# Performance work log

Hardware: AMD Instinct MI355X
Metric: run time of the kernel (lower is better)

Reference implementation:

```python
import jax, jax.numpy as jnp
import numpy as np

TOP_K = 2


def setup_inputs() -> dict:
    key = jax.random.key(0)
    ks = jax.random.split(key, 8)
    B, S, H, I, E = 1, 1024, 2048, 1408, 8
    s = 0.02  # init scale for weights
    return {
        "hidden_states": jax.random.normal(ks[0], (B, S, H), jnp.float32),
        "gate_weight": jax.random.normal(ks[1], (E, H), jnp.float32) * s,
        "expert_gate_w": jax.random.normal(ks[2], (E, I, H), jnp.float32) * s,
        "expert_up_w": jax.random.normal(ks[3], (E, I, H), jnp.float32) * s,
        "expert_down_w": jax.random.normal(ks[4], (E, H, I), jnp.float32) * s,
        "shared_gate_w": jax.random.normal(ks[5], (I, H), jnp.float32) * s,
        "shared_up_w": jax.random.normal(ks[6], (I, H), jnp.float32) * s,
        "shared_down_w": jax.random.normal(ks[7], (H, I), jnp.float32) * s,
    }


def reference(hidden_states, gate_weight, expert_gate_w, expert_up_w, expert_down_w,
              shared_gate_w, shared_up_w, shared_down_w):
    B, S, H = hidden_states.shape
    E = gate_weight.shape[0]
    x = hidden_states.reshape(-1, H)          # [T, H]
    T = x.shape[0]

    # --- gate: top-k routing (e_score_correction_bias buffer is zeros -> no-op) ---
    logits = x @ gate_weight.T                # [T, E]
    topk_logits, topk_idx = jax.lax.top_k(logits, TOP_K)
    topk_w = jax.nn.softmax(topk_logits, axis=-1)  # [T, K]

    # per-token per-expert combine weight (0 for non-selected experts) [T, E]
    comb = jnp.zeros((T, E), x.dtype).at[jnp.arange(T)[:, None], topk_idx].add(topk_w)

    # --- routed experts: dense over E, weighted combine (mathematically identical
    # to the per-token loop since comb==0 for unselected experts) ---
    g = jnp.einsum('th,eih->tei', x, expert_gate_w)   # [T, E, I]
    u = jnp.einsum('th,eih->tei', x, expert_up_w)     # [T, E, I]
    h = jax.nn.silu(g) * u                            # [T, E, I]
    y = jnp.einsum('tei,ehi->teh', h, expert_down_w)  # [T, E, H]
    out = jnp.einsum('teh,te->th', y, comb)           # [T, H]

    # --- shared expert ---
    sh = (jax.nn.silu(x @ shared_gate_w.T) * (x @ shared_up_w.T)) @ shared_down_w.T
    out = out + sh
    return out.reshape(B, S, H)
```

## Files before the change

kernel.cpp:

```cpp
#include <hip/hip_runtime.h>
#include <hip/hip_bf16.h>

typedef unsigned short u16;
typedef __bf16 bf16x8 __attribute__((ext_vector_type(8)));
typedef float f32x4 __attribute__((ext_vector_type(4)));

#define H_DIM 2048
#define I_DIM 1408
#define T_TOK 1024
#define NEXP 8
#define LS 40

__device__ __forceinline__ u16 f2bf(float f) {
    union { float f; unsigned u; } v; v.f = f;
    unsigned r = v.u + 0x7FFFu + ((v.u >> 16) & 1u);
    return (u16)(r >> 16);
}
__device__ __forceinline__ unsigned pack2(float a, float b) {
    float2 t; t.x = a; t.y = b;
    __hip_bfloat162 h = __float22bfloat162_rn(t);
    union { __hip_bfloat162 h; unsigned u; } v; v.h = h;
    return v.u;
}
__device__ __forceinline__ uint2 pack4(float4 f) {
    uint2 r; r.x = pack2(f.x, f.y); r.y = pack2(f.z, f.w); return r;
}

__global__ __launch_bounds__(256)
void router_kernel(const float* __restrict__ x, const float* __restrict__ gw,
                   int* __restrict__ counts, int* __restrict__ tok, float* __restrict__ tw) {
    int wave = threadIdx.x >> 6;
    int lane = threadIdx.x & 63;
    int t = blockIdx.x * 4 + wave;
    const float* xr = x + (size_t)t * H_DIM;
    float acc[NEXP];
#pragma unroll
    for (int e = 0; e < NEXP; e++) acc[e] = 0.f;
    for (int h = lane; h < H_DIM; h += 64) {
        float xv = xr[h];
#pragma unroll
        for (int e = 0; e < NEXP; e++) acc[e] += xv * gw[e * H_DIM + h];
    }
#pragma unroll
    for (int e = 0; e < NEXP; e++) {
#pragma unroll
        for (int off = 32; off > 0; off >>= 1) acc[e] += __shfl_xor(acc[e], off);
    }
    if (lane == 0) {
        int i0 = 0; float v0 = acc[0];
#pragma unroll
        for (int e = 1; e < NEXP; e++) if (acc[e] > v0) { v0 = acc[e]; i0 = e; }
        int i1 = -1; float v1 = -3.0e38f;
#pragma unroll
        for (int e = 0; e < NEXP; e++) if (e != i0 && acc[e] > v1) { v1 = acc[e]; i1 = e; }
        float ex = __expf(v1 - v0);
        float w0 = 1.f / (1.f + ex);
        float w1 = 1.f - w0;
        int s0 = atomicAdd(&counts[i0], 1);
        tok[i0 * T_TOK + s0] = t; tw[i0 * T_TOK + s0] = w0;
        int s1 = atomicAdd(&counts[i1], 1);
        tok[i1 * T_TOK + s1] = t; tw[i1 * T_TOK + s1] = w1;
    }
}

__global__ __launch_bounds__(256, 2)
void gate_up_kernel(const float* __restrict__ x,
                    const float* __restrict__ egw, const float* __restrict__ euw,
                    const float* __restrict__ sgw, const float* __restrict__ suw,
                    const int* __restrict__ counts, const int* __restrict__ tok,
                    const float* __restrict__ tw,
                    u16* __restrict__ h_r, u16* __restrict__ h_s) {
    __shared__ u16 lA[64 * LS];
    __shared__ u16 lG[128 * LS];
    __shared__ u16 lU[128 * LS];

    int e = blockIdx.z;
    bool routed = (e < NEXP);
    int cnt, hbase;
    const float *Wg, *Wu; u16* hout;
    if (routed) {
        cnt = counts[e];
        int p = 0;
#pragma unroll
        for (int i = 0; i < NEXP; i++) { int c = counts[i]; if (i < e) p += c; }
        hbase = p;
        Wg = egw + (size_t)e * I_DIM * H_DIM;
        Wu = euw + (size_t)e * I_DIM * H_DIM;
        hout = h_r;
    } else {
        cnt = T_TOK; hbase = 0; Wg = sgw; Wu = suw; hout = h_s;
    }
    int m0 = blockIdx.y * 64;
    if (m0 >= cnt) return;
    int n0 = blockIdx.x * 128;

    int tid = threadIdx.x;
    int lane = tid & 63;
    int w = tid >> 6;

    const float* ap[2]; int sa[2];
#pragma unroll
    for (int i = 0; i < 2; i++) {
        int slot = tid + i * 256;
        int row = slot >> 3, c4 = slot & 7;
        sa[i] = row * LS + c4 * 4;
        int trow = m0 + row; if (trow > cnt - 1) trow = cnt - 1;
        int tix = routed ? tok[e * T_TOK + trow] : trow;
        ap[i] = x + (size_t)tix * H_DIM + c4 * 4;
    }
    const float* gp[4]; const float* up[4]; int sg[4];
#pragma unroll
    for (int i = 0; i < 4; i++) {
        int slot = tid + i * 256;
        int row = slot >> 3, c4 = slot & 7;
        sg[i] = row * LS + c4 * 4;
        gp[i] = Wg + (size_t)(n0 + row) * H_DIM + c4 * 4;
        up[i] = Wu + (size_t)(n0 + row) * H_DIM + c4 * 4;
    }

    f32x4 zero = {0.f, 0.f, 0.f, 0.f};
    f32x4 accg[4][2], accu[4][2];
#pragma unroll
    for (int a = 0; a < 4; a++)
#pragma unroll
        for (int b = 0; b < 2; b++) { accg[a][b] = zero; accu[a][b] = zero; }

    int r16 = lane & 15, kq = lane >> 4;

    float4 ra[2], rg[4], ru[4];
#pragma unroll
    for (int i = 0; i < 2; i++) ra[i] = *(const float4*)(ap[i]);
#pragma unroll
    for (int i = 0; i < 4; i++) { rg[i] = *(const float4*)(gp[i]); ru[i] = *(const float4*)(up[i]); }

    for (int k0 = 0; k0 < H_DIM; k0 += 32) {
#pragma unroll
        for (int i = 0; i < 2; i++) *(uint2*)&lA[sa[i]] = pack4(ra[i]);
#pragma unroll
        for (int i = 0; i < 4; i++) {
            *(uint2*)&lG[sg[i]] = pack4(rg[i]);
            *(uint2*)&lU[sg[i]] = pack4(ru[i]);
        }
        __syncthreads();
        if (k0 + 32 < H_DIM) {
            int kn = k0 + 32;
#pragma unroll
            for (int i = 0; i < 2; i++) ra[i] = *(const float4*)(ap[i] + kn);
#pragma unroll
            for (int i = 0; i < 4; i++) { rg[i] = *(const float4*)(gp[i] + kn); ru[i] = *(const float4*)(up[i] + kn); }
        }
        bf16x8 af[4], gf[2], uf[2];
#pragma unroll
        for (int mi = 0; mi < 4; mi++)
            af[mi] = *(const bf16x8*)&lA[(mi * 16 + r16) * LS + kq * 8];
#pragma unroll
        for (int ni = 0; ni < 2; ni++) {
            gf[ni] = *(const bf16x8*)&lG[(w * 32 + ni * 16 + r16) * LS + kq * 8];
            uf[ni] = *(const bf16x8*)&lU[(w * 32 + ni * 16 + r16) * LS + kq * 8];
        }
#pragma unroll
        for (int mi = 0; mi < 4; mi++)
#pragma unroll
            for (int ni = 0; ni < 2; ni++) {
                accg[mi][ni] = __builtin_amdgcn_mfma_f32_16x16x32_bf16(af[mi], gf[ni], accg[mi][ni], 0, 0, 0);
                accu[mi][ni] = __builtin_amdgcn_mfma_f32_16x16x32_bf16(af[mi], uf[ni], accu[mi][ni], 0, 0, 0);
            }
        __syncthreads();
    }

#pragma unroll
    for (int mi = 0; mi < 4; mi++) {
#pragma unroll
        for (int r = 0; r < 4; r++) {
            int row = mi * 16 + kq * 4 + r;
            int gr = m0 + row;
            if (gr < cnt) {
                float wt = routed ? tw[e * T_TOK + gr] : 1.0f;
                u16* hrow = hout + (size_t)(hbase + gr) * I_DIM + n0 + w * 32;
#pragma unroll
                for (int ni = 0; ni < 2; ni++) {
                    float g = accg[mi][ni][r], u = accu[mi][ni][r];
                    float hv = (g / (1.f + __expf(-g))) * u * wt;
                    hrow[ni * 16 + r16] = f2bf(hv);
                }
            }
        }
    }
}

__global__ __launch_bounds__(256, 2)
void down_kernel(const u16* __restrict__ h_r, const u16* __restrict__ h_s,
                 const float* __restrict__ edw, const float* __restrict__ sdw,
                 const int* __restrict__ counts, const int* __restrict__ tok,
                 float* __restrict__ out) {
    __shared__ u16 lA[64 * LS];
    __shared__ u16 lB[128 * LS];

    int e = blockIdx.z;
    bool routed = (e < NEXP);
    int cnt, hbase;
    const float* Wd; const u16* hin;
    if (routed) {
        cnt = counts[e];
        int p = 0;
#pragma unroll
        for (int i = 0; i < NEXP; i++) { int c = counts[i]; if (i < e) p += c; }
        hbase = p;
        Wd = edw + (size_t)e * H_DIM * I_DIM;
        hin = h_r;
    } else {
        cnt = T_TOK; hbase = 0; Wd = sdw; hin = h_s;
    }
    int m0 = blockIdx.y * 64;
    if (m0 >= cnt) return;
    int n0 = blockIdx.x * 128;

    int tid = threadIdx.x;
    int lane = tid & 63;
    int w = tid >> 6;

    int arow = tid >> 2, ac8 = tid & 3;
    int hr = m0 + arow; if (hr > cnt - 1) hr = cnt - 1;
    const u16* ap = hin + (size_t)(hbase + hr) * I_DIM + ac8 * 8;
    int sa = arow * LS + ac8 * 8;
    const float* bp[4]; int sb[4];
#pragma unroll
    for (int i = 0; i < 4; i++) {
        int slot = tid + i * 256;
        int row = slot >> 3, c4 = slot & 7;
        bp[i] = Wd + (size_t)(n0 + row) * I_DIM + c4 * 4;
        sb[i] = row * LS + c4 * 4;
    }

    f32x4 zero = {0.f, 0.f, 0.f, 0.f};
    f32x4 acc[4][2];
#pragma unroll
    for (int a = 0; a < 4; a++)
#pragma unroll
        for (int b = 0; b < 2; b++) acc[a][b] = zero;

    int r16 = lane & 15, kq = lane >> 4;

    uint4 ra = *(const uint4*)(ap);
    float4 rb[4];
#pragma unroll
    for (int i = 0; i < 4; i++) rb[i] = *(const float4*)(bp[i]);

    for (int k0 = 0; k0 < I_DIM; k0 += 32) {
        *(uint4*)&lA[sa] = ra;
#pragma unroll
        for (int i = 0; i < 4; i++) *(uint2*)&lB[sb[i]] = pack4(rb[i]);
        __syncthreads();
        if (k0 + 32 < I_DIM) {
            int kn = k0 + 32;
            ra = *(const uint4*)(ap + kn);
#pragma unroll
            for (int i = 0; i < 4; i++) rb[i] = *(const float4*)(bp[i] + kn);
        }
        bf16x8 af[4], bfr[2];
#pragma unroll
        for (int mi = 0; mi < 4; mi++)
            af[mi] = *(const bf16x8*)&lA[(mi * 16 + r16) * LS + kq * 8];
#pragma unroll
        for (int ni = 0; ni < 2; ni++)
            bfr[ni] = *(const bf16x8*)&lB[(w * 32 + ni * 16 + r16) * LS + kq * 8];
#pragma unroll
        for (int mi = 0; mi < 4; mi++)
#pragma unroll
            for (int ni = 0; ni < 2; ni++)
                acc[mi][ni] = __builtin_amdgcn_mfma_f32_16x16x32_bf16(af[mi], bfr[ni], acc[mi][ni], 0, 0, 0);
        __syncthreads();
    }

#pragma unroll
    for (int mi = 0; mi < 4; mi++) {
#pragma unroll
        for (int r = 0; r < 4; r++) {
            int row = mi * 16 + kq * 4 + r;
            int gr = m0 + row;
            if (gr < cnt) {
                int t = routed ? tok[e * T_TOK + gr] : gr;
                float* orow = out + (size_t)t * H_DIM + n0 + w * 32;
#pragma unroll
                for (int ni = 0; ni < 2; ni++)
                    atomicAdd(&orow[ni * 16 + r16], acc[mi][ni][r]);
            }
        }
    }
}

extern "C" void kernel_launch(void* const* d_in, const int* in_sizes, int n_in,
                              void* d_out, int out_size, void* d_ws, size_t ws_size,
                              hipStream_t stream) {
    const float* x   = (const float*)d_in[0];
    const float* gw  = (const float*)d_in[1];
    const float* egw = (const float*)d_in[2];
    const float* euw = (const float*)d_in[3];
    const float* edw = (const float*)d_in[4];
    const float* sgw = (const float*)d_in[5];
    const float* suw = (const float*)d_in[6];
    const float* sdw = (const float*)d_in[7];
    float* out = (float*)d_out;

    char* ws = (char*)d_ws;
    int*   counts = (int*)ws;
    int*   tok    = (int*)(ws + 256);
    float* tw     = (float*)(ws + 256 + 32768);
    u16*   h_r    = (u16*)(ws + 65792);
    u16*   h_s    = h_r + (size_t)2048 * I_DIM;

    hipMemsetAsync(counts, 0, 32, stream);
    hipMemsetAsync(out, 0, (size_t)T_TOK * H_DIM * sizeof(float), stream);
    router_kernel<<<256, 256, 0, stream>>>(x, gw, counts, tok, tw);
    gate_up_kernel<<<dim3(11, 16, 9), 256, 0, stream>>>(x, egw, euw, sgw, suw, counts, tok, tw, h_r, h_s);
    down_kernel<<<dim3(16, 16, 9), 256, 0, stream>>>(h_r, h_s, edw, sdw, counts, tok, out);
}
```

Measured before the change: 543.2 us.

## Pre-convert weights to bf16 and stage GEMM tiles via direct global-to-LDS loads

Adds a conversion kernel that casts all expert and shared weights plus activations to bf16 in workspace every call. New gate/up and down kernels then load bf16 tiles straight into LDS with global_load_lds, using an XOR-swizzled layout and K=64 steps, and target 3 blocks per CU. The intent is to halve the bytes the GEMMs read and remove the per-tile register conversion. The cost is an extra full pass that reads the fp32 weights and writes bf16 copies, which may cancel the saving because the weights are only used once per call. The old fp32 path stays as a fallback when the workspace is too small.

New measurement: 523.7 us. 1.04x faster.

```diff
diff --git a/kernel.cpp b/kernel.cpp
--- a/kernel.cpp
+++ b/kernel.cpp
@@ -24,6 +24,10 @@
 }
 __device__ __forceinline__ uint2 pack4(float4 f) {
     uint2 r; r.x = pack2(f.x, f.y); r.y = pack2(f.z, f.w); return r;
+}
+__device__ __forceinline__ void g2l16(const void* g, void* l) {
+    __builtin_amdgcn_global_load_lds((const __attribute__((address_space(1))) void*)g,
+                                     (__attribute__((address_space(3))) void*)l, 16, 0, 0);
 }
 
 __global__ __launch_bounds__(256)
@@ -63,21 +67,35 @@
     }
 }
 
-__global__ __launch_bounds__(256, 2)
-void gate_up_kernel(const float* __restrict__ x,
-                    const float* __restrict__ egw, const float* __restrict__ euw,
-                    const float* __restrict__ sgw, const float* __restrict__ suw,
-                    const int* __restrict__ counts, const int* __restrict__ tok,
-                    const float* __restrict__ tw,
-                    u16* __restrict__ h_r, u16* __restrict__ h_s) {
-    __shared__ u16 lA[64 * LS];
-    __shared__ u16 lG[128 * LS];
-    __shared__ u16 lU[128 * LS];
+struct Cvt7 { const float* in[7]; u16* out[7]; int nchunk[7]; };
+__global__ __launch_bounds__(256)
+void convert_bf(Cvt7 a) {
+    int z = blockIdx.z;
+    int n = a.nchunk[z];
+    const float* in = a.in[z]; u16* out = a.out[z];
+    for (int i = blockIdx.x * 256 + threadIdx.x; i < n; i += gridDim.x * 256) {
+        const float4* p = (const float4*)(in + (size_t)i * 8);
+        float4 f0 = p[0], f1 = p[1];
+        uint4 o; o.x = pack2(f0.x, f0.y); o.y = pack2(f0.z, f0.w);
+        o.z = pack2(f1.x, f1.y); o.w = pack2(f1.z, f1.w);
+        *(uint4*)(out + (size_t)i * 8) = o;
+    }
+}
+
+__global__ __launch_bounds__(256, 3)
+void gate_up_bf(const u16* __restrict__ xb,
+                const u16* __restrict__ egw, const u16* __restrict__ euw,
+                const u16* __restrict__ sgw, const u16* __restrict__ suw,
+                const int* __restrict__ counts, const int* __restrict__ tok,
+                const float* __restrict__ tw,
+                u16* __restrict__ h_r, u16* __restrict__ h_s) {
+    __shared__ u16 lA[64 * 64];
+    __shared__ u16 lG[128 * 64];
+    __shared__ u16 lU[128 * 64];
 
     int e = blockIdx.z;
     bool routed = (e < NEXP);
-    int cnt, hbase;
-    const float *Wg, *Wu; u16* hout;
+    int cnt, hbase; const u16 *Wg, *Wu; u16* hout;
     if (routed) {
         cnt = counts[e];
         int p = 0;
@@ -87,17 +105,225 @@
         Wg = egw + (size_t)e * I_DIM * H_DIM;
         Wu = euw + (size_t)e * I_DIM * H_DIM;
         hout = h_r;
-    } else {
-        cnt = T_TOK; hbase = 0; Wg = sgw; Wu = suw; hout = h_s;
-    }
+    } else { cnt = T_TOK; hbase = 0; Wg = sgw; Wu = suw; hout = h_s; }
     int m0 = blockIdx.y * 64;
     if (m0 >= cnt) return;
     int n0 = blockIdx.x * 128;
 
-    int tid = threadIdx.x;
-    int lane = tid & 63;
-    int w = tid >> 6;
-
+    int tid = threadIdx.x, lane = tid & 63, w = tid >> 6;
+
+    const u16* aptr[2]; u16* alds[2];
+#pragma unroll
+    for (int j = 0; j < 2; j++) {
+        int chunk = w * 128 + j * 64 + lane;
+        int row = chunk >> 3, cl = chunk & 7;
+        int cg = cl ^ (row & 7);
+        int trow = m0 + row; if (trow > cnt - 1) trow = cnt - 1;
+        int tix = routed ? tok[e * T_TOK + trow] : trow;
+        aptr[j] = xb + (size_t)tix * H_DIM + cg * 8;
+        alds[j] = &lA[(w * 128 + j * 64) * 8];
+    }
+    const u16* gptr[4]; const u16* uptr[4]; u16* glds[4]; u16* ulds[4];
+#pragma unroll
+    for (int j = 0; j < 4; j++) {
+        int chunk = w * 256 + j * 64 + lane;
+        int row = chunk >> 3, cl = chunk & 7;
+        int cg = cl ^ (row & 7);
+        gptr[j] = Wg + (size_t)(n0 + row) * H_DIM + cg * 8;
+        uptr[j] = Wu + (size_t)(n0 + row) * H_DIM + cg * 8;
+        glds[j] = &lG[(w * 256 + j * 64) * 8];
+        ulds[j] = &lU[(w * 256 + j * 64) * 8];
+    }
+
+    f32x4 zero = {0.f, 0.f, 0.f, 0.f};
+    f32x4 accg[4][2], accu[4][2];
+#pragma unroll
+    for (int a = 0; a < 4; a++)
+#pragma unroll
+        for (int b = 0; b < 2; b++) { accg[a][b] = zero; accu[a][b] = zero; }
+
+    int r16 = lane & 15, q = lane >> 4;
+
+    for (int k0 = 0; k0 < H_DIM; k0 += 64) {
+#pragma unroll
+        for (int j = 0; j < 2; j++) g2l16(aptr[j] + k0, alds[j]);
+#pragma unroll
+        for (int j = 0; j < 4; j++) { g2l16(gptr[j] + k0, glds[j]); g2l16(uptr[j] + k0, ulds[j]); }
+        __syncthreads();
+#pragma unroll
+        for (int kh = 0; kh < 2; kh++) {
+            bf16x8 af[4], gf[2], uf[2];
+#pragma unroll
+            for (int mi = 0; mi < 4; mi++) {
+                int row = mi * 16 + r16;
+                int ch = (kh * 4 + q) ^ (row & 7);
+                af[mi] = *(const bf16x8*)&lA[row * 64 + ch * 8];
+            }
+#pragma unroll
+            for (int ni = 0; ni < 2; ni++) {
+                int row = w * 32 + ni * 16 + r16;
+                int ch = (kh * 4 + q) ^ (row & 7);
+                gf[ni] = *(const bf16x8*)&lG[row * 64 + ch * 8];
+                uf[ni] = *(const bf16x8*)&lU[row * 64 + ch * 8];
+            }
+#pragma unroll
+            for (int mi = 0; mi < 4; mi++)
+#pragma unroll
+                for (int ni = 0; ni < 2; ni++) {
+                    accg[mi][ni] = __builtin_amdgcn_mfma_f32_16x16x32_bf16(af[mi], gf[ni], accg[mi][ni], 0, 0, 0);
+                    accu[mi][ni] = __builtin_amdgcn_mfma_f32_16x16x32_bf16(af[mi], uf[ni], accu[mi][ni], 0, 0, 0);
+                }
+        }
+        __syncthreads();
+    }
+
+#pragma unroll
+    for (int mi = 0; mi < 4; mi++) {
+#pragma unroll
+        for (int r = 0; r < 4; r++) {
+            int row = mi * 16 + q * 4 + r;
+            int gr = m0 + row;
+            if (gr < cnt) {
+                float wt = routed ? tw[e * T_TOK + gr] : 1.0f;
+                u16* hrow = hout + (size_t)(hbase + gr) * I_DIM + n0 + w * 32;
+#pragma unroll
+                for (int ni = 0; ni < 2; ni++) {
+                    float g = accg[mi][ni][r], u = accu[mi][ni][r];
+                    float hv = (g / (1.f + __expf(-g))) * u * wt;
+                    hrow[ni * 16 + r16] = f2bf(hv);
+                }
+            }
+        }
+    }
+}
+
+__global__ __launch_bounds__(256, 3)
+void down_bf(const u16* __restrict__ h_r, const u16* __restrict__ h_s,
+             const u16* __restrict__ edw, const u16* __restrict__ sdw,
+             const int* __restrict__ counts, const int* __restrict__ tok,
+             float* __restrict__ out) {
+    __shared__ u16 lA[64 * 64];
+    __shared__ u16 lB[128 * 64];
+
+    int e = blockIdx.z;
+    bool routed = (e < NEXP);
+    int cnt, hbase; const u16* Wd; const u16* hin;
+    if (routed) {
+        cnt = counts[e];
+        int p = 0;
+#pragma unroll
+        for (int i = 0; i < NEXP; i++) { int c = counts[i]; if (i < e) p += c; }
+        hbase = p;
+        Wd = edw + (size_t)e * H_DIM * I_DIM;
+        hin = h_r;
+    } else { cnt = T_TOK; hbase = 0; Wd = sdw; hin = h_s; }
+    int m0 = blockIdx.y * 64;
+    if (m0 >= cnt) return;
+    int n0 = blockIdx.x * 128;
+
+    int tid = threadIdx.x, lane = tid & 63, w = tid >> 6;
+
+    const u16* aptr[2]; u16* alds[2];
+#pragma unroll
+    for (int j = 0; j < 2; j++) {
+        int chunk = w * 128 + j * 64 + lane;
+        int row = chunk >> 3, cl = chunk & 7;
+        int cg = cl ^ (row & 7);
+        int hr = m0 + row; if (hr > cnt - 1) hr = cnt - 1;
+        aptr[j] = hin + (size_t)(hbase + hr) * I_DIM + cg * 8;
+        alds[j] = &lA[(w * 128 + j * 64) * 8];
+    }
+    const u16* bptr[4]; u16* blds[4];
+#pragma unroll
+    for (int j = 0; j < 4; j++) {
+        int chunk = w * 256 + j * 64 + lane;
+        int row = chunk >> 3, cl = chunk & 7;
+        int cg = cl ^ (row & 7);
+        bptr[j] = Wd + (size_t)(n0 + row) * I_DIM + cg * 8;
+        blds[j] = &lB[(w * 256 + j * 64) * 8];
+    }
+
+    f32x4 zero = {0.f, 0.f, 0.f, 0.f};
+    f32x4 acc[4][2];
+#pragma unroll
+    for (int a = 0; a < 4; a++)
+#pragma unroll
+        for (int b = 0; b < 2; b++) acc[a][b] = zero;
+
+    int r16 = lane & 15, q = lane >> 4;
+
+    for (int k0 = 0; k0 < I_DIM; k0 += 64) {
+#pragma unroll
+        for (int j = 0; j < 2; j++) g2l16(aptr[j] + k0, alds[j]);
+#pragma unroll
+        for (int j = 0; j < 4; j++) g2l16(bptr[j] + k0, blds[j]);
+        __syncthreads();
+#pragma unroll
+        for (int kh = 0; kh < 2; kh++) {
+            bf16x8 af[4], bfr[2];
+#pragma unroll
+            for (int mi = 0; mi < 4; mi++) {
+                int row = mi * 16 + r16;
+                int ch = (kh * 4 + q) ^ (row & 7);
+                af[mi] = *(const bf16x8*)&lA[row * 64 + ch * 8];
+            }
+#pragma unroll
+            for (int ni = 0; ni < 2; ni++) {
+                int row = w * 32 + ni * 16 + r16;
+                int ch = (kh * 4 + q) ^ (row & 7);
+                bfr[ni] = *(const bf16x8*)&lB[row * 64 + ch * 8];
+            }
+#pragma unroll
+            for (int mi = 0; mi < 4; mi++)
+#pragma unroll
+                for (int ni = 0; ni < 2; ni++)
+                    acc[mi][ni] = __builtin_amdgcn_mfma_f32_16x16x32_bf16(af[mi], bfr[ni], acc[mi][ni], 0, 0, 0);
+        }
+        __syncthreads();
+    }
+
+#pragma unroll
+    for (int mi = 0; mi < 4; mi++) {
+#pragma unroll
+        for (int r = 0; r < 4; r++) {
+            int row = mi * 16 + q * 4 + r;
+            int gr = m0 + row;
+            if (gr < cnt) {
+                int t = routed ? tok[e * T_TOK + gr] : gr;
+                float* orow = out + (size_t)t * H_DIM + n0 + w * 32;
+#pragma unroll
+                for (int ni = 0; ni < 2; ni++)
+                    atomicAdd(&orow[ni * 16 + r16], acc[mi][ni][r]);
+            }
+        }
+    }
+}
+
+__global__ __launch_bounds__(256, 2)
+void gate_up_f32(const float* __restrict__ x,
+                 const float* __restrict__ egw, const float* __restrict__ euw,
+                 const float* __restrict__ sgw, const float* __restrict__ suw,
+                 const int* __restrict__ counts, const int* __restrict__ tok,
+                 const float* __restrict__ tw,
+                 u16* __restrict__ h_r, u16* __restrict__ h_s) {
+    __shared__ u16 lA[64 * LS];
+    __shared__ u16 lG[128 * LS];
+    __shared__ u16 lU[128 * LS];
+    int e = blockIdx.z;
+    bool routed = (e < NEXP);
+    int cnt, hbase; const float *Wg, *Wu; u16* hout;
+    if (routed) {
+        cnt = counts[e];
+        int p = 0;
+#pragma unroll
+        for (int i = 0; i < NEXP; i++) { int c = counts[i]; if (i < e) p += c; }
+        hbase = p;
+        Wg = egw + (size_t)e * I_DIM * H_DIM; Wu = euw + (size_t)e * I_DIM * H_DIM; hout = h_r;
+    } else { cnt = T_TOK; hbase = 0; Wg = sgw; Wu = suw; hout = h_s; }
+    int m0 = blockIdx.y * 64;
+    if (m0 >= cnt) return;
+    int n0 = blockIdx.x * 128;
+    int tid = threadIdx.x, lane = tid & 63, w = tid >> 6;
     const float* ap[2]; int sa[2];
 #pragma unroll
     for (int i = 0; i < 2; i++) {
@@ -117,30 +343,23 @@
         gp[i] = Wg + (size_t)(n0 + row) * H_DIM + c4 * 4;
         up[i] = Wu + (size_t)(n0 + row) * H_DIM + c4 * 4;
     }
-
     f32x4 zero = {0.f, 0.f, 0.f, 0.f};
     f32x4 accg[4][2], accu[4][2];
 #pragma unroll
     for (int a = 0; a < 4; a++)
 #pragma unroll
         for (int b = 0; b < 2; b++) { accg[a][b] = zero; accu[a][b] = zero; }
-
     int r16 = lane & 15, kq = lane >> 4;
-
     float4 ra[2], rg[4], ru[4];
 #pragma unroll
     for (int i = 0; i < 2; i++) ra[i] = *(const float4*)(ap[i]);
 #pragma unroll
     for (int i = 0; i < 4; i++) { rg[i] = *(const float4*)(gp[i]); ru[i] = *(const float4*)(up[i]); }
-
     for (int k0 = 0; k0 < H_DIM; k0 += 32) {
 #pragma unroll
         for (int i = 0; i < 2; i++) *(uint2*)&lA[sa[i]] = pack4(ra[i]);
 #pragma unroll
-        for (int i = 0; i < 4; i++) {
-            *(uint2*)&lG[sg[i]] = pack4(rg[i]);
-            *(uint2*)&lU[sg[i]] = pack4(ru[i]);
-        }
+        for (int i = 0; i < 4; i++) { *(uint2*)&lG[sg[i]] = pack4(rg[i]); *(uint2*)&lU[sg[i]] = pack4(ru[i]); }
         __syncthreads();
         if (k0 + 32 < H_DIM) {
             int kn = k0 + 32;
@@ -151,8 +370,7 @@
         }
         bf16x8 af[4], gf[2], uf[2];
 #pragma unroll
-        for (int mi = 0; mi < 4; mi++)
-            af[mi] = *(const bf16x8*)&lA[(mi * 16 + r16) * LS + kq * 8];
+        for (int mi = 0; mi < 4; mi++) af[mi] = *(const bf16x8*)&lA[(mi * 16 + r16) * LS + kq * 8];
 #pragma unroll
         for (int ni = 0; ni < 2; ni++) {
             gf[ni] = *(const bf16x8*)&lG[(w * 32 + ni * 16 + r16) * LS + kq * 8];
@@ -167,7 +385,6 @@
             }
         __syncthreads();
     }
-
 #pragma unroll
     for (int mi = 0; mi < 4; mi++) {
 #pragma unroll
@@ -189,36 +406,27 @@
 }
 
 __global__ __launch_bounds__(256, 2)
-void down_kernel(const u16* __restrict__ h_r, const u16* __restrict__ h_s,
-                 const float* __restrict__ edw, const float* __restrict__ sdw,
-                 const int* __restrict__ counts, const int* __restrict__ tok,
-                 float* __restrict__ out) {
+void down_f32(const u16* __restrict__ h_r, const u16* __restrict__ h_s,
+              const float* __restrict__ edw, const float* __restrict__ sdw,
+              const int* __restrict__ counts, const int* __restrict__ tok,
+              float* __restrict__ out) {
     __shared__ u16 lA[64 * LS];
     __shared__ u16 lB[128 * LS];
-
     int e = blockIdx.z;
     bool routed = (e < NEXP);
-    int cnt, hbase;
-    const float* Wd; const u16* hin;
+    int cnt, hbase; const float* Wd; const u16* hin;
     if (routed) {
         cnt = counts[e];
         int p = 0;
 #pragma unroll
         for (int i = 0; i < NEXP; i++) { int c = counts[i]; if (i < e) p += c; }
         hbase = p;
-        Wd = edw + (size_t)e * H_DIM * I_DIM;
-        hin = h_r;
-    } else {
-        cnt = T_TOK; hbase = 0; Wd = sdw; hin = h_s;
-    }
+        Wd = edw + (size_t)e * H_DIM * I_DIM; hin = h_r;
+    } else { cnt = T_TOK; hbase = 0; Wd = sdw; hin = h_s; }
     int m0 = blockIdx.y * 64;
     if (m0 >= cnt) return;
     int n0 = blockIdx.x * 128;
-
-    int tid = threadIdx.x;
-    int lane = tid & 63;
-    int w = tid >> 6;
-
+    int tid = threadIdx.x, lane = tid & 63, w = tid >> 6;
     int arow = tid >> 2, ac8 = tid & 3;
     int hr = m0 + arow; if (hr > cnt - 1) hr = cnt - 1;
     const u16* ap = hin + (size_t)(hbase + hr) * I_DIM + ac8 * 8;
@@ -231,21 +439,17 @@
         bp[i] = Wd + (size_t)(n0 + row) * I_DIM + c4 * 4;
         sb[i] = row * LS + c4 * 4;
     }
-
     f32x4 zero = {0.f, 0.f, 0.f, 0.f};
     f32x4 acc[4][2];
 #pragma unroll
     for (int a = 0; a < 4; a++)
 #pragma unroll
         for (int b = 0; b < 2; b++) acc[a][b] = zero;
-
     int r16 = lane & 15, kq = lane >> 4;
-
     uint4 ra = *(const uint4*)(ap);
     float4 rb[4];
 #pragma unroll
     for (int i = 0; i < 4; i++) rb[i] = *(const float4*)(bp[i]);
-
     for (int k0 = 0; k0 < I_DIM; k0 += 32) {
         *(uint4*)&lA[sa] = ra;
 #pragma unroll
@@ -259,11 +463,9 @@
         }
         bf16x8 af[4], bfr[2];
 #pragma unroll
-        for (int mi = 0; mi < 4; mi++)
-            af[mi] = *(const bf16x8*)&lA[(mi * 16 + r16) * LS + kq * 8];
-#pragma unroll
-        for (int ni = 0; ni < 2; ni++)
-            bfr[ni] = *(const bf16x8*)&lB[(w * 32 + ni * 16 + r16) * LS + kq * 8];
+        for (int mi = 0; mi < 4; mi++) af[mi] = *(const bf16x8*)&lA[(mi * 16 + r16) * LS + kq * 8];
+#pragma unroll
+        for (int ni = 0; ni < 2; ni++) bfr[ni] = *(const bf16x8*)&lB[(w * 32 + ni * 16 + r16) * LS + kq * 8];
 #pragma unroll
         for (int mi = 0; mi < 4; mi++)
 #pragma unroll
@@ -271,7 +473,6 @@
                 acc[mi][ni] = __builtin_amdgcn_mfma_f32_16x16x32_bf16(af[mi], bfr[ni], acc[mi][ni], 0, 0, 0);
         __syncthreads();
     }
-
 #pragma unroll
     for (int mi = 0; mi < 4; mi++) {
 #pragma unroll
@@ -312,6 +513,29 @@
     hipMemsetAsync(counts, 0, 32, stream);
     hipMemsetAsync(out, 0, (size_t)T_TOK * H_DIM * sizeof(float), stream);
     router_kernel<<<256, 256, 0, stream>>>(x, gw, counts, tok, tw);
-    gate_up_kernel<<<dim3(11, 16, 9), 256, 0, stream>>>(x, egw, euw, sgw, suw, counts, tok, tw, h_r, h_s);
-    down_kernel<<<dim3(16, 16, 9), 256, 0, stream>>>(h_r, h_s, edw, sdw, counts, tok, out);
-}
+
+    const size_t NEED = 168624384ull;
+    if (ws_size >= NEED) {
+        u16* xbf = (u16*)(ws + 8716544);
+        u16* egb = (u16*)(ws + 12910848);
+        u16* eub = (u16*)(ws + 59048192);
+        u16* edb = (u16*)(ws + 105185536);
+        u16* sgb = (u16*)(ws + 151322880);
+        u16* sub = (u16*)(ws + 157090048);
+        u16* sdb = (u16*)(ws + 162857216);
+        Cvt7 c;
+        c.in[0] = egw; c.out[0] = egb; c.nchunk[0] = 2883584;
+        c.in[1] = euw; c.out[1] = eub; c.nchunk[1] = 2883584;
+        c.in[2] = edw; c.out[2] = edb; c.nchunk[2] = 2883584;
+        c.in[3] = sgw; c.out[3] = sgb; c.nchunk[3] = 360448;
+        c.in[4] = suw; c.out[4] = sub; c.nchunk[4] = 360448;
+        c.in[5] = sdw; c.out[5] = sdb; c.nchunk[5] = 360448;
+        c.in[6] = x;   c.out[6] = xbf; c.nchunk[6] = 262144;
+        convert_bf<<<dim3(2048, 1, 7), 256, 0, stream>>>(c);
+        gate_up_bf<<<dim3(11, 16, 9), 256, 0, stream>>>(xbf, egb, eub, sgb, sub, counts, tok, tw, h_r, h_s);
+        down_bf<<<dim3(16, 16, 9), 256, 0, stream>>>(h_r, h_s, edb, sdb, counts, tok, out);
+    } else {
+        gate_up_f32<<<dim3(11, 16, 9), 256, 0, stream>>>(x, egw, euw, sgw, suw, counts, tok, tw, h_r, h_s);
+        down_f32<<<dim3(16, 16, 9), 256, 0, stream>>>(h_r, h_s, edw, sdw, counts, tok, out);
+    }
+}
```
